# Optimization experiments

Measured on AMD Instinct MI355X. Metric: run time of the kernel, lower is better.

The kernel has to match this reference:

```python
import jax, jax.numpy as jnp
import numpy as np

jax.config.update("jax_enable_x64", True)

N = 100000   # active sparse sites
H = W = 512  # event-camera grid
CIN, CMID, COUT = 64, 384, 64
SHIFT = 16   # shift_n


def setup_inputs() -> dict:
    rng = np.random.default_rng(0)
    # unique active coordinates on the grid (batch index 0)
    flat = rng.permutation(H * W)[:N]
    ys, xs = flat // W, flat % W
    # dense index map with 1-pixel halo; sentinel N = missing neighbor
    idx_map = np.full((H + 2, W + 2), N, dtype=np.int32)
    idx_map[ys + 1, xs + 1] = np.arange(N, dtype=np.int32)
    # 3x3 neighborhood indices per active site, row-major kernel order
    nbr = np.stack([idx_map[ys + 1 + dy, xs + 1 + dx]
                    for dy in (-1, 0, 1) for dx in (-1, 0, 1)], axis=1)

    def ri(lo, hi, shape):
        return jnp.asarray(rng.integers(lo, hi, size=shape), dtype=jnp.float32)

    return {
        "feats": ri(-128, 128, (N, CIN)),      # int8-valued input features
        "w1": ri(-128, 128, (CIN, CMID)),       # 1x1 expand weights
        "b1": ri(-1024, 1024, (CMID,)),
        "s1": ri(1, 16, (CMID,)),
        "w_dw": ri(-128, 128, (9, CMID)),       # 3x3 depthwise weights [k, C]
        "b2": ri(-1024, 1024, (CMID,)),
        "s2": ri(1, 64, (CMID,)),
        "w3": ri(-128, 128, (CMID, COUT)),      # 1x1 project weights
        "b3": ri(-1024, 1024, (COUT,)),
        "s3": ri(1, 16, (COUT,)),
        "neighbor_idx": jnp.asarray(nbr),       # [N, 9] int32, N = sentinel
    }


def _quant(psum, bias, scale, relu):
    # (psum + bias) * scale, add 2^(shift-1), arithmetic >> shift,
    # clamp to int8 range, optional relu. psum values are exact integers.
    t = psum.astype(jnp.int64)
    t = ((t + bias.astype(jnp.int64)) * scale.astype(jnp.int64)
         + (1 << (SHIFT - 1))) >> SHIFT
    y = jnp.clip(t.astype(jnp.float32), -128.0, 127.0)
    return jnp.maximum(y, 0.0) if relu else y


def reference(feats, w1, b1, s1, w_dw, b2, s2, w3, b3, s3, neighbor_idx):
    # 1x1 expand (sparse 1x1 conv == matmul over active sites) + quant + relu
    x1 = _quant(feats @ w1, b1, s1, True)                       # [N, CMID]
    # 3x3 depthwise sparse conv: gather 9 neighbors (zero row for missing)
    pad = jnp.concatenate([x1, jnp.zeros((1, x1.shape[1]), x1.dtype)], axis=0)
    psum2 = jnp.einsum('nkc,kc->nc', pad[neighbor_idx], w_dw)   # [N, CMID]
    x2 = _quant(psum2, b2, s2, True)
    # 1x1 project + quant (linear bottleneck: no relu)
    x3 = _quant(x2 @ w3, b3, s3, False)                          # [N, COUT]
    return x3
```

## Files before the change

### kernel.cpp

```cpp
#include <hip/hip_runtime.h>
#include <stdint.h>

#define N_SITES 100000
#define NPAD    100032
#define CIN 64
#define CMID 384
#define COUT 64
#define SHIFT 16

typedef int  v4i __attribute__((ext_vector_type(4)));
typedef unsigned int v4u __attribute__((ext_vector_type(4)));

__global__ __launch_bounds__(256) void pack_feats(const float* __restrict__ f,
                                                  int8_t* __restrict__ o) {
    int i = blockIdx.x * 256 + threadIdx.x;
    if (i >= N_SITES * CIN / 4) return;
    const float4 v = ((const float4*)f)[i];
    uint32_t w = (uint32_t)(uint8_t)(int8_t)__float2int_rn(v.x)
               | ((uint32_t)(uint8_t)(int8_t)__float2int_rn(v.y) << 8)
               | ((uint32_t)(uint8_t)(int8_t)__float2int_rn(v.z) << 16)
               | ((uint32_t)(uint8_t)(int8_t)__float2int_rn(v.w) << 24);
    ((uint32_t*)o)[i] = w;
}

__global__ __launch_bounds__(256) void pack_weights(
    const float* __restrict__ w1, const float* __restrict__ w3,
    const float* __restrict__ b1, const float* __restrict__ s1,
    const float* __restrict__ b2, const float* __restrict__ s2,
    const float* __restrict__ b3, const float* __restrict__ s3,
    const float* __restrict__ wdw,
    int8_t* __restrict__ w1p, int8_t* __restrict__ w3p,
    int* __restrict__ q1, int* __restrict__ q3,
    int8_t* __restrict__ wdw8, int* __restrict__ bs2,
    int8_t* __restrict__ x1s)
{
    int o = blockIdx.x * 256 + threadIdx.x;
    if (o < 24 * 64 * 16) {
        int t = o >> 10, l = (o >> 4) & 63, b = o & 15;
        int k = ((l >> 4) << 4) + b;
        int col = t * 16 + (l & 15);
        w1p[o] = (int8_t)__float2int_rn(w1[k * CMID + col]);
    }
    int o3 = o - 24 * 64 * 16;
    if (o3 >= 0 && o3 < 6 * 4 * 64 * 16) {
        int ks = o3 >> 12, t = (o3 >> 10) & 3;
        int l = (o3 >> 4) & 63, b = o3 & 15;
        int k = ks * 64 + ((l >> 4) << 4) + b;
        int col = t * 16 + (l & 15);
        w3p[o3] = (int8_t)__float2int_rn(w3[k * COUT + col]);
    }
    if (o < 9 * CMID)
        wdw8[o] = (int8_t)__float2int_rn(wdw[o]);
    if (o < CMID) {
        q1[o] = __float2int_rn(b1[o]);
        q1[CMID + o] = __float2int_rn(s1[o]);
        int bb = __float2int_rn(b2[o]);
        int ss = __float2int_rn(s2[o]);
        bs2[o] = (bb & 0xFFFF) | (ss << 16);
        x1s[(size_t)N_SITES * CMID + o] = 0;
    }
    if (o < COUT) {
        q3[o] = __float2int_rn(b3[o]);
        q3[COUT + o] = __float2int_rn(s3[o]);
    }
}

__global__ __launch_bounds__(256) void k1_mfma(
    const int8_t* __restrict__ feats8, const int8_t* __restrict__ w1p,
    const int* __restrict__ q1, int8_t* __restrict__ x1s)
{
    const int lane = threadIdx.x & 63;
    const int wave = threadIdx.x >> 6;
    const int site0 = blockIdx.x * 64 + wave * 16;
    const int row0 = site0 + ((lane >> 4) << 2);
    const v4i a = *(const v4i*)(feats8 + (size_t)(site0 + (lane & 15)) * CIN
                                + ((lane >> 4) << 4));
    const v4i* bp = (const v4i*)w1p + lane;
#pragma unroll
    for (int t = 0; t < 24; ++t) {
        v4i b = bp[t * 64];
        v4i acc = {0, 0, 0, 0};
        acc = __builtin_amdgcn_mfma_i32_16x16x64_i8(a, b, acc, 0, 0, 0);
        const int col = t * 16 + (lane & 15);
        const int bi = q1[col], si = q1[CMID + col];
#pragma unroll
        for (int r = 0; r < 4; ++r) {
            int site = row0 + r;
            if (site < N_SITES) {
                int v = (acc[r] + bi) * si + (1 << (SHIFT - 1));
                v >>= SHIFT;
                v = max(0, min(127, v));
                x1s[(size_t)site * CMID + col] = (int8_t)v;
            }
        }
    }
}

__global__ __launch_bounds__(256) void k2_dw(
    const int8_t* __restrict__ x1s, const int* __restrict__ nbr,
    const int8_t* __restrict__ wdw8, const int* __restrict__ bs2,
    int8_t* __restrict__ x2s)
{
    const int g = blockIdx.x * 256 + threadIdx.x;
    const int site = g / 24;
    const int c0 = (g - site * 24) << 4;

    const int* nb = &nbr[site * 9];
    int idx[9];
#pragma unroll
    for (int k = 0; k < 9; ++k) idx[k] = nb[k];

    v4u V[9];
#pragma unroll
    for (int k = 0; k < 9; ++k) {
        const int off = (idx[k] << 8) + (idx[k] << 7) + c0;
        V[k] = *(const v4u*)(x1s + off);
    }

    int acc[16];
#pragma unroll
    for (int j = 0; j < 16; ++j) acc[j] = 0;

#pragma unroll
    for (int k = 0; k < 9; ++k) {
        const v4u W = *(const v4u*)(wdw8 + k * CMID + c0);
#pragma unroll
        for (int j = 0; j < 4; ++j) {
#pragma unroll
            for (int b = 0; b < 4; ++b) {
                const int v = (int)(uint8_t)(V[k][j] >> (8 * b));
                const int w = (int)(int8_t)(W[j] >> (8 * b));
                acc[j * 4 + b] += v * w;
            }
        }
    }

    const v4i BS0 = *(const v4i*)(bs2 + c0);
    const v4i BS1 = *(const v4i*)(bs2 + c0 + 4);
    const v4i BS2 = *(const v4i*)(bs2 + c0 + 8);
    const v4i BS3 = *(const v4i*)(bs2 + c0 + 12);
    const v4i BS[4] = {BS0, BS1, BS2, BS3};

    v4u outw;
#pragma unroll
    for (int j = 0; j < 4; ++j) {
        uint32_t wrd = 0;
#pragma unroll
        for (int b = 0; b < 4; ++b) {
            const int bsv = BS[j][b];
            const int bb = (bsv << 16) >> 16;
            const int ss = bsv >> 16;
            int t = ((acc[j * 4 + b] + bb) * ss + (1 << (SHIFT - 1))) >> SHIFT;
            t = max(0, min(127, t));
            wrd |= (uint32_t)t << (8 * b);
        }
        outw[j] = wrd;
    }
    *(v4u*)(x2s + (site << 8) + (site << 7) + c0) = outw;
}

__global__ __launch_bounds__(256) void k3_mfma(
    const int8_t* __restrict__ x2s, const int8_t* __restrict__ w3p,
    const int* __restrict__ q3, float* __restrict__ out)
{
    const int lane = threadIdx.x & 63;
    const int wave = threadIdx.x >> 6;
    const int site0 = blockIdx.x * 64 + wave * 16;
    const int row0 = site0 + ((lane >> 4) << 2);
    const int8_t* xbase = x2s + (size_t)(site0 + (lane & 15)) * CMID
                          + ((lane >> 4) << 4);
    v4i acc[4] = {{0,0,0,0},{0,0,0,0},{0,0,0,0},{0,0,0,0}};
#pragma unroll
    for (int ks = 0; ks < 6; ++ks) {
        v4i a = *(const v4i*)(xbase + ks * 64);
#pragma unroll
        for (int t = 0; t < 4; ++t) {
            v4i b = *((const v4i*)w3p + (ks * 4 + t) * 64 + lane);
            acc[t] = __builtin_amdgcn_mfma_i32_16x16x64_i8(a, b, acc[t], 0, 0, 0);
        }
    }
#pragma unroll
    for (int t = 0; t < 4; ++t) {
        const int col = t * 16 + (lane & 15);
        const int bo = q3[col], so = q3[COUT + col];
#pragma unroll
        for (int r = 0; r < 4; ++r) {
            int site = row0 + r;
            if (site < N_SITES) {
                int v = (acc[t][r] + bo) * so + (1 << (SHIFT - 1));
                v >>= SHIFT;
                v = max(-128, min(127, v));
                out[(size_t)site * COUT + col] = (float)v;
            }
        }
    }
}

extern "C" void kernel_launch(void* const* d_in, const int* in_sizes, int n_in,
                              void* d_out, int out_size, void* d_ws, size_t ws_size,
                              hipStream_t stream) {
    const float* feats = (const float*)d_in[0];
    const float* w1    = (const float*)d_in[1];
    const float* b1    = (const float*)d_in[2];
    const float* s1    = (const float*)d_in[3];
    const float* wdw   = (const float*)d_in[4];
    const float* b2    = (const float*)d_in[5];
    const float* s2    = (const float*)d_in[6];
    const float* w3    = (const float*)d_in[7];
    const float* b3    = (const float*)d_in[8];
    const float* s3    = (const float*)d_in[9];
    const int*   nbr   = (const int*)d_in[10];
    float* out = (float*)d_out;

    int8_t* x1s    = (int8_t*)d_ws;
    int8_t* x2s    = x1s + (size_t)NPAD * CMID;
    int8_t* feats8 = x2s;
    int8_t* w1p    = x2s + (size_t)NPAD * CMID;
    int8_t* w3p    = w1p + 24 * 64 * 16;
    int*    q1     = (int*)(w3p + 6 * 4 * 64 * 16);
    int*    q3     = q1 + 2 * CMID;
    int8_t* wdw8   = (int8_t*)(q3 + 2 * COUT);
    int*    bs2    = (int*)(wdw8 + 9 * CMID);

    pack_feats<<<(N_SITES * CIN / 4 + 255) / 256, 256, 0, stream>>>(feats, feats8);
    pack_weights<<<192, 256, 0, stream>>>(w1, w3, b1, s1, b2, s2, b3, s3, wdw,
                                          w1p, w3p, q1, q3, wdw8, bs2, x1s);
    k1_mfma<<<NPAD / 64, 256, 0, stream>>>(feats8, w1p, q1, x1s);
    k2_dw<<<N_SITES * 24 / 256, 256, 0, stream>>>(x1s, nbr, wdw8, bs2, x2s);
    k3_mfma<<<NPAD / 64, 256, 0, stream>>>(x2s, w3p, q3, out);
}
```

Before: 90.75 us.

## Fuse feature packing into expand GEMM and depthwise into project GEMM via LDS

Removes the separate feature-pack kernel: the expand kernel now reads float features directly, converts them to int8, and swaps the MFMA operand roles so each lane writes packed 4-byte output words instead of single bytes. The depthwise conv and the 1x1 project are fused into one 384-thread kernel. That kernel stages the 64-site x2 tile in shared memory and keeps 4 sites per thread to reuse the depthwise weights, which are now held as int32. This drops the x2 round trip through global memory and one launch, at the cost of higher register pressure and only 4 of 6 waves doing the MFMA phase.

```diff
diff --git a/kernel.cpp b/kernel.cpp
--- a/kernel.cpp
+++ b/kernel.cpp
@@ -8,20 +8,9 @@
 #define COUT 64
 #define SHIFT 16
 
-typedef int  v4i __attribute__((ext_vector_type(4)));
+typedef int   v4i __attribute__((ext_vector_type(4)));
 typedef unsigned int v4u __attribute__((ext_vector_type(4)));
-
-__global__ __launch_bounds__(256) void pack_feats(const float* __restrict__ f,
-                                                  int8_t* __restrict__ o) {
-    int i = blockIdx.x * 256 + threadIdx.x;
-    if (i >= N_SITES * CIN / 4) return;
-    const float4 v = ((const float4*)f)[i];
-    uint32_t w = (uint32_t)(uint8_t)(int8_t)__float2int_rn(v.x)
-               | ((uint32_t)(uint8_t)(int8_t)__float2int_rn(v.y) << 8)
-               | ((uint32_t)(uint8_t)(int8_t)__float2int_rn(v.z) << 16)
-               | ((uint32_t)(uint8_t)(int8_t)__float2int_rn(v.w) << 24);
-    ((uint32_t*)o)[i] = w;
-}
+typedef float v4f __attribute__((ext_vector_type(4)));
 
 __global__ __launch_bounds__(256) void pack_weights(
     const float* __restrict__ w1, const float* __restrict__ w3,
@@ -31,7 +20,7 @@
     const float* __restrict__ wdw,
     int8_t* __restrict__ w1p, int8_t* __restrict__ w3p,
     int* __restrict__ q1, int* __restrict__ q3,
-    int8_t* __restrict__ wdw8, int* __restrict__ bs2,
+    int* __restrict__ wdw32, int* __restrict__ bs2,
     int8_t* __restrict__ x1s)
 {
     int o = blockIdx.x * 256 + threadIdx.x;
@@ -50,7 +39,7 @@
         w3p[o3] = (int8_t)__float2int_rn(w3[k * COUT + col]);
     }
     if (o < 9 * CMID)
-        wdw8[o] = (int8_t)__float2int_rn(wdw[o]);
+        wdw32[o] = __float2int_rn(wdw[o]);
     if (o < CMID) {
         q1[o] = __float2int_rn(b1[o]);
         q1[CMID + o] = __float2int_rn(s1[o]);
@@ -65,132 +54,163 @@
     }
 }
 
-__global__ __launch_bounds__(256) void k1_mfma(
-    const int8_t* __restrict__ feats8, const int8_t* __restrict__ w1p,
+__global__ __launch_bounds__(256) void k1f(
+    const float* __restrict__ feats, const int8_t* __restrict__ w1p,
     const int* __restrict__ q1, int8_t* __restrict__ x1s)
 {
     const int lane = threadIdx.x & 63;
     const int wave = threadIdx.x >> 6;
-    const int site0 = blockIdx.x * 64 + wave * 16;
-    const int row0 = site0 + ((lane >> 4) << 2);
-    const v4i a = *(const v4i*)(feats8 + (size_t)(site0 + (lane & 15)) * CIN
-                                + ((lane >> 4) << 4));
-    const v4i* bp = (const v4i*)w1p + lane;
+    const int site = blockIdx.x * 64 + wave * 16 + (lane & 15);
+    const int rsite = min(site, N_SITES - 1);
+    const bool ok = site < N_SITES;
+    const int kbase = (lane >> 4) << 4;
+    const int cbase = (lane >> 4) << 2;
+
+    v4i b;
+    const float* fp = feats + (size_t)rsite * CIN + kbase;
+#pragma unroll
+    for (int j = 0; j < 4; ++j) {
+        v4f f = *(const v4f*)(fp + 4 * j);
+        uint32_t pk = (uint32_t)(__float2int_rn(f[0]) & 255)
+                    | ((uint32_t)(__float2int_rn(f[1]) & 255) << 8)
+                    | ((uint32_t)(__float2int_rn(f[2]) & 255) << 16)
+                    | ((uint32_t)__float2int_rn(f[3]) << 24);
+        b[j] = (int)pk;
+    }
+
+    const v4i* ap = (const v4i*)w1p + lane;
+    int8_t* orow = x1s + (size_t)site * CMID;
 #pragma unroll
     for (int t = 0; t < 24; ++t) {
-        v4i b = bp[t * 64];
+        v4i a = ap[t * 64];
         v4i acc = {0, 0, 0, 0};
         acc = __builtin_amdgcn_mfma_i32_16x16x64_i8(a, b, acc, 0, 0, 0);
-        const int col = t * 16 + (lane & 15);
-        const int bi = q1[col], si = q1[CMID + col];
+        const int co = t * 16 + cbase;
+        const v4i bi = *(const v4i*)(q1 + co);
+        const v4i si = *(const v4i*)(q1 + CMID + co);
+        uint32_t wrd = 0;
 #pragma unroll
         for (int r = 0; r < 4; ++r) {
-            int site = row0 + r;
-            if (site < N_SITES) {
-                int v = (acc[r] + bi) * si + (1 << (SHIFT - 1));
-                v >>= SHIFT;
-                v = max(0, min(127, v));
-                x1s[(size_t)site * CMID + col] = (int8_t)v;
-            }
-        }
-    }
-}
-
-__global__ __launch_bounds__(256) void k2_dw(
+            int v = (__mul24(acc[r] + bi[r], si[r]) + (1 << (SHIFT - 1))) >> SHIFT;
+            v = max(0, min(127, v));
+            wrd |= (uint32_t)v << (8 * r);
+        }
+        if (ok) *(uint32_t*)(orow + co) = wrd;
+    }
+}
+
+__global__ __launch_bounds__(384) void k23(
     const int8_t* __restrict__ x1s, const int* __restrict__ nbr,
-    const int8_t* __restrict__ wdw8, const int* __restrict__ bs2,
-    int8_t* __restrict__ x2s)
+    const int* __restrict__ wdw32, const int* __restrict__ bs2,
+    const int8_t* __restrict__ w3p, const int* __restrict__ q3,
+    float* __restrict__ out)
 {
-    const int g = blockIdx.x * 256 + threadIdx.x;
-    const int site = g / 24;
-    const int c0 = (g - site * 24) << 4;
-
-    const int* nb = &nbr[site * 9];
-    int idx[9];
-#pragma unroll
-    for (int k = 0; k < 9; ++k) idx[k] = nb[k];
-
-    v4u V[9];
-#pragma unroll
-    for (int k = 0; k < 9; ++k) {
-        const int off = (idx[k] << 8) + (idx[k] << 7) + c0;
-        V[k] = *(const v4u*)(x1s + off);
-    }
-
-    int acc[16];
-#pragma unroll
-    for (int j = 0; j < 16; ++j) acc[j] = 0;
-
-#pragma unroll
-    for (int k = 0; k < 9; ++k) {
-        const v4u W = *(const v4u*)(wdw8 + k * CMID + c0);
-#pragma unroll
-        for (int j = 0; j < 4; ++j) {
-#pragma unroll
-            for (int b = 0; b < 4; ++b) {
-                const int v = (int)(uint8_t)(V[k][j] >> (8 * b));
-                const int w = (int)(int8_t)(W[j] >> (8 * b));
-                acc[j * 4 + b] += v * w;
-            }
-        }
-    }
-
-    const v4i BS0 = *(const v4i*)(bs2 + c0);
-    const v4i BS1 = *(const v4i*)(bs2 + c0 + 4);
-    const v4i BS2 = *(const v4i*)(bs2 + c0 + 8);
-    const v4i BS3 = *(const v4i*)(bs2 + c0 + 12);
-    const v4i BS[4] = {BS0, BS1, BS2, BS3};
-
-    v4u outw;
-#pragma unroll
-    for (int j = 0; j < 4; ++j) {
-        uint32_t wrd = 0;
-#pragma unroll
-        for (int b = 0; b < 4; ++b) {
-            const int bsv = BS[j][b];
-            const int bb = (bsv << 16) >> 16;
-            const int ss = bsv >> 16;
-            int t = ((acc[j * 4 + b] + bb) * ss + (1 << (SHIFT - 1))) >> SHIFT;
-            t = max(0, min(127, t));
-            wrd |= (uint32_t)t << (8 * b);
-        }
-        outw[j] = wrd;
-    }
-    *(v4u*)(x2s + (site << 8) + (site << 7) + c0) = outw;
-}
-
-__global__ __launch_bounds__(256) void k3_mfma(
-    const int8_t* __restrict__ x2s, const int8_t* __restrict__ w3p,
-    const int* __restrict__ q3, float* __restrict__ out)
-{
-    const int lane = threadIdx.x & 63;
-    const int wave = threadIdx.x >> 6;
-    const int site0 = blockIdx.x * 64 + wave * 16;
-    const int row0 = site0 + ((lane >> 4) << 2);
-    const int8_t* xbase = x2s + (size_t)(site0 + (lane & 15)) * CMID
-                          + ((lane >> 4) << 4);
-    v4i acc[4] = {{0,0,0,0},{0,0,0,0},{0,0,0,0},{0,0,0,0}};
-#pragma unroll
-    for (int ks = 0; ks < 6; ++ks) {
-        v4i a = *(const v4i*)(xbase + ks * 64);
-#pragma unroll
-        for (int t = 0; t < 4; ++t) {
-            v4i b = *((const v4i*)w3p + (ks * 4 + t) * 64 + lane);
-            acc[t] = __builtin_amdgcn_mfma_i32_16x16x64_i8(a, b, acc[t], 0, 0, 0);
-        }
-    }
-#pragma unroll
-    for (int t = 0; t < 4; ++t) {
-        const int col = t * 16 + (lane & 15);
-        const int bo = q3[col], so = q3[COUT + col];
-#pragma unroll
-        for (int r = 0; r < 4; ++r) {
-            int site = row0 + r;
-            if (site < N_SITES) {
-                int v = (acc[t][r] + bo) * so + (1 << (SHIFT - 1));
-                v >>= SHIFT;
-                v = max(-128, min(127, v));
-                out[(size_t)site * COUT + col] = (float)v;
+    __shared__ int8_t xt[64][400];
+    const int site0 = blockIdx.x * 64;
+    const int tid = threadIdx.x;
+
+    {
+        const int c0  = (tid % 24) * 16;
+        const int slb = tid / 24;
+
+        int idx[4][9];
+#pragma unroll
+        for (int s = 0; s < 4; ++s) {
+            const int sc = min(site0 + slb + s * 16, N_SITES - 1);
+            const int* nb = nbr + (size_t)sc * 9;
+#pragma unroll
+            for (int k = 0; k < 9; ++k) idx[s][k] = nb[k];
+        }
+
+        int acc[4][16];
+#pragma unroll
+        for (int s = 0; s < 4; ++s)
+#pragma unroll
+            for (int j = 0; j < 16; ++j) acc[s][j] = 0;
+
+#pragma unroll
+        for (int k = 0; k < 9; ++k) {
+            int W[16];
+#pragma unroll
+            for (int j = 0; j < 4; ++j) {
+                v4i w4 = *(const v4i*)(wdw32 + k * CMID + c0 + 4 * j);
+#pragma unroll
+                for (int b = 0; b < 4; ++b) W[j * 4 + b] = w4[b];
+            }
+#pragma unroll
+            for (int s = 0; s < 4; ++s) {
+                const v4u V = *(const v4u*)(x1s + (size_t)idx[s][k] * CMID + c0);
+#pragma unroll
+                for (int j = 0; j < 4; ++j)
+#pragma unroll
+                    for (int b = 0; b < 4; ++b) {
+                        const int v = (int)((V[j] >> (8 * b)) & 0xff);
+                        acc[s][j * 4 + b] += __mul24(v, W[j * 4 + b]);
+                    }
+            }
+        }
+
+        v4i BS[4];
+#pragma unroll
+        for (int j = 0; j < 4; ++j) BS[j] = *(const v4i*)(bs2 + c0 + 4 * j);
+
+#pragma unroll
+        for (int s = 0; s < 4; ++s) {
+            v4u ow;
+#pragma unroll
+            for (int j = 0; j < 4; ++j) {
+                uint32_t wrd = 0;
+#pragma unroll
+                for (int b = 0; b < 4; ++b) {
+                    const int bsv = BS[j][b];
+                    const int bb = (int)(int16_t)(bsv & 0xFFFF);
+                    const int ss = bsv >> 16;
+                    int t = (__mul24(acc[s][j * 4 + b] + bb, ss)
+                             + (1 << (SHIFT - 1))) >> SHIFT;
+                    t = max(0, min(127, t));
+                    wrd |= (uint32_t)t << (8 * b);
+                }
+                ow[j] = wrd;
+            }
+            *(v4u*)(&xt[slb + s * 16][c0]) = ow;
+        }
+    }
+    __syncthreads();
+
+    const int wv = tid >> 6;
+    if (wv < 4) {
+        const int lane = tid & 63;
+        const int sl = wv * 16 + (lane & 15);
+        const int site = site0 + sl;
+        const int kb = (lane >> 4) << 4;
+        const int cb = (lane >> 4) << 2;
+
+        v4i acc3[4] = {{0,0,0,0},{0,0,0,0},{0,0,0,0},{0,0,0,0}};
+#pragma unroll
+        for (int ks = 0; ks < 6; ++ks) {
+            const v4i bfr = *(const v4i*)(&xt[sl][ks * 64 + kb]);
+#pragma unroll
+            for (int t = 0; t < 4; ++t) {
+                const v4i afr = *((const v4i*)w3p + (ks * 4 + t) * 64 + lane);
+                acc3[t] = __builtin_amdgcn_mfma_i32_16x16x64_i8(afr, bfr, acc3[t], 0, 0, 0);
+            }
+        }
+        if (site < N_SITES) {
+            float* orow = out + (size_t)site * COUT;
+#pragma unroll
+            for (int t = 0; t < 4; ++t) {
+                const int co = t * 16 + cb;
+                const v4i bo = *(const v4i*)(q3 + co);
+                const v4i so = *(const v4i*)(q3 + COUT + co);
+                v4f o;
+#pragma unroll
+                for (int r = 0; r < 4; ++r) {
+                    int v = (__mul24(acc3[t][r] + bo[r], so[r])
+                             + (1 << (SHIFT - 1))) >> SHIFT;
+                    v = max(-128, min(127, v));
+                    o[r] = (float)v;
+                }
+                *(v4f*)(orow + co) = o;
             }
         }
     }
@@ -212,20 +232,16 @@
     const int*   nbr   = (const int*)d_in[10];
     float* out = (float*)d_out;
 
-    int8_t* x1s    = (int8_t*)d_ws;
-    int8_t* x2s    = x1s + (size_t)NPAD * CMID;
-    int8_t* feats8 = x2s;
-    int8_t* w1p    = x2s + (size_t)NPAD * CMID;
-    int8_t* w3p    = w1p + 24 * 64 * 16;
-    int*    q1     = (int*)(w3p + 6 * 4 * 64 * 16);
-    int*    q3     = q1 + 2 * CMID;
-    int8_t* wdw8   = (int8_t*)(q3 + 2 * COUT);
-    int*    bs2    = (int*)(wdw8 + 9 * CMID);
-
-    pack_feats<<<(N_SITES * CIN / 4 + 255) / 256, 256, 0, stream>>>(feats, feats8);
+    int8_t* x1s   = (int8_t*)d_ws;
+    int8_t* w1p   = x1s + (size_t)(NPAD + 64) * CMID;
+    int8_t* w3p   = w1p + 24 * 64 * 16;
+    int*    q1    = (int*)(w3p + 6 * 4 * 64 * 16);
+    int*    q3    = q1 + 2 * CMID;
+    int*    wdw32 = q3 + 2 * COUT;
+    int*    bs2   = wdw32 + 9 * CMID;
+
     pack_weights<<<192, 256, 0, stream>>>(w1, w3, b1, s1, b2, s2, b3, s3, wdw,
-                                          w1p, w3p, q1, q3, wdw8, bs2, x1s);
-    k1_mfma<<<NPAD / 64, 256, 0, stream>>>(feats8, w1p, q1, x1s);
-    k2_dw<<<N_SITES * 24 / 256, 256, 0, stream>>>(x1s, nbr, wdw8, bs2, x2s);
-    k3_mfma<<<NPAD / 64, 256, 0, stream>>>(x2s, w3p, q3, out);
-}
+                                          w1p, w3p, q1, q3, wdw32, bs2, x1s);
+    k1f<<<NPAD / 64, 256, 0, stream>>>(feats, w1p, q1, x1s);
+    k23<<<NPAD / 64, 384, 0, stream>>>(x1s, nbr, wdw32, bs2, w3p, q3, out);
+}
```

Result: slower. 122.8 us (+35.3%).

## Merge pack kernels and use packed sdot4 in depthwise kernel

Applied to the files above, without the earlier changes.

Folds the feature-packing and weight-packing kernels into a single launch, removing one kernel launch and its gap. The depthwise kernel now keeps its weights pre-packed four taps per word. It uses byte permutes plus sdot4 to do four neighbor multiply-adds per instruction instead of scalar byte-extract multiplies. Bias and scale are stored unpacked, and __mul24 is used for the requantize step. This adds dependence on sdot4 builtin availability, with a scalar fallback, and relies on x1 values being non-negative int8 for signed dot correctness.

```diff
diff --git a/kernel.cpp b/kernel.cpp
--- a/kernel.cpp
+++ b/kernel.cpp
@@ -8,33 +8,43 @@
 #define COUT 64
 #define SHIFT 16
 
-typedef int  v4i __attribute__((ext_vector_type(4)));
+#define FEAT_BLOCKS 6250
+
+typedef int   v4i __attribute__((ext_vector_type(4)));
 typedef unsigned int v4u __attribute__((ext_vector_type(4)));
 
-__global__ __launch_bounds__(256) void pack_feats(const float* __restrict__ f,
-                                                  int8_t* __restrict__ o) {
-    int i = blockIdx.x * 256 + threadIdx.x;
-    if (i >= N_SITES * CIN / 4) return;
-    const float4 v = ((const float4*)f)[i];
-    uint32_t w = (uint32_t)(uint8_t)(int8_t)__float2int_rn(v.x)
-               | ((uint32_t)(uint8_t)(int8_t)__float2int_rn(v.y) << 8)
-               | ((uint32_t)(uint8_t)(int8_t)__float2int_rn(v.z) << 16)
-               | ((uint32_t)(uint8_t)(int8_t)__float2int_rn(v.w) << 24);
-    ((uint32_t*)o)[i] = w;
-}
-
-__global__ __launch_bounds__(256) void pack_weights(
+#if __has_builtin(__builtin_amdgcn_sdot4)
+#define HAS_SDOT4 1
+#else
+#define HAS_SDOT4 0
+#endif
+
+__global__ __launch_bounds__(256) void pack_all(
+    const float* __restrict__ feats,
     const float* __restrict__ w1, const float* __restrict__ w3,
     const float* __restrict__ b1, const float* __restrict__ s1,
     const float* __restrict__ b2, const float* __restrict__ s2,
     const float* __restrict__ b3, const float* __restrict__ s3,
     const float* __restrict__ wdw,
+    int8_t* __restrict__ feats8,
     int8_t* __restrict__ w1p, int8_t* __restrict__ w3p,
     int* __restrict__ q1, int* __restrict__ q3,
-    int8_t* __restrict__ wdw8, int* __restrict__ bs2,
+    int* __restrict__ wp03, int* __restrict__ wp47, int* __restrict__ w8,
+    int* __restrict__ q2b, int* __restrict__ q2s,
     int8_t* __restrict__ x1s)
 {
-    int o = blockIdx.x * 256 + threadIdx.x;
+    if (blockIdx.x < FEAT_BLOCKS) {
+        int i = blockIdx.x * 256 + threadIdx.x;
+        if (i >= N_SITES * CIN / 4) return;
+        const float4 v = ((const float4*)feats)[i];
+        uint32_t w = (uint32_t)(uint8_t)(int8_t)__float2int_rn(v.x)
+                   | ((uint32_t)(uint8_t)(int8_t)__float2int_rn(v.y) << 8)
+                   | ((uint32_t)(uint8_t)(int8_t)__float2int_rn(v.z) << 16)
+                   | ((uint32_t)(uint8_t)(int8_t)__float2int_rn(v.w) << 24);
+        ((uint32_t*)feats8)[i] = w;
+        return;
+    }
+    int o = (blockIdx.x - FEAT_BLOCKS) * 256 + threadIdx.x;
     if (o < 24 * 64 * 16) {
         int t = o >> 10, l = (o >> 4) & 63, b = o & 15;
         int k = ((l >> 4) << 4) + b;
@@ -49,14 +59,21 @@
         int col = t * 16 + (l & 15);
         w3p[o3] = (int8_t)__float2int_rn(w3[k * COUT + col]);
     }
-    if (o < 9 * CMID)
-        wdw8[o] = (int8_t)__float2int_rn(wdw[o]);
     if (o < CMID) {
+        uint32_t p03 = 0, p47 = 0;
+#pragma unroll
+        for (int k = 0; k < 4; ++k)
+            p03 |= (uint32_t)(uint8_t)(int8_t)__float2int_rn(wdw[k * CMID + o]) << (8 * k);
+#pragma unroll
+        for (int k = 0; k < 4; ++k)
+            p47 |= (uint32_t)(uint8_t)(int8_t)__float2int_rn(wdw[(k + 4) * CMID + o]) << (8 * k);
+        wp03[o] = (int)p03;
+        wp47[o] = (int)p47;
+        w8[o]   = __float2int_rn(wdw[8 * CMID + o]);
+        q2b[o]  = __float2int_rn(b2[o]);
+        q2s[o]  = __float2int_rn(s2[o]);
         q1[o] = __float2int_rn(b1[o]);
         q1[CMID + o] = __float2int_rn(s1[o]);
-        int bb = __float2int_rn(b2[o]);
-        int ss = __float2int_rn(s2[o]);
-        bs2[o] = (bb & 0xFFFF) | (ss << 16);
         x1s[(size_t)N_SITES * CMID + o] = 0;
     }
     if (o < COUT) {
@@ -98,65 +115,69 @@
 
 __global__ __launch_bounds__(256) void k2_dw(
     const int8_t* __restrict__ x1s, const int* __restrict__ nbr,
-    const int8_t* __restrict__ wdw8, const int* __restrict__ bs2,
-    int8_t* __restrict__ x2s)
+    const int* __restrict__ wp03, const int* __restrict__ wp47,
+    const int* __restrict__ w8, const int* __restrict__ q2b,
+    const int* __restrict__ q2s, int8_t* __restrict__ x2s)
 {
     const int g = blockIdx.x * 256 + threadIdx.x;
     const int site = g / 24;
     const int c0 = (g - site * 24) << 4;
 
-    const int* nb = &nbr[site * 9];
+    const int* nb = nbr + (size_t)site * 9;
     int idx[9];
 #pragma unroll
     for (int k = 0; k < 9; ++k) idx[k] = nb[k];
 
     v4u V[9];
 #pragma unroll
-    for (int k = 0; k < 9; ++k) {
-        const int off = (idx[k] << 8) + (idx[k] << 7) + c0;
-        V[k] = *(const v4u*)(x1s + off);
-    }
-
-    int acc[16];
-#pragma unroll
-    for (int j = 0; j < 16; ++j) acc[j] = 0;
-
-#pragma unroll
-    for (int k = 0; k < 9; ++k) {
-        const v4u W = *(const v4u*)(wdw8 + k * CMID + c0);
-#pragma unroll
-        for (int j = 0; j < 4; ++j) {
-#pragma unroll
-            for (int b = 0; b < 4; ++b) {
-                const int v = (int)(uint8_t)(V[k][j] >> (8 * b));
-                const int w = (int)(int8_t)(W[j] >> (8 * b));
-                acc[j * 4 + b] += v * w;
-            }
-        }
-    }
-
-    const v4i BS0 = *(const v4i*)(bs2 + c0);
-    const v4i BS1 = *(const v4i*)(bs2 + c0 + 4);
-    const v4i BS2 = *(const v4i*)(bs2 + c0 + 8);
-    const v4i BS3 = *(const v4i*)(bs2 + c0 + 12);
-    const v4i BS[4] = {BS0, BS1, BS2, BS3};
+    for (int k = 0; k < 9; ++k)
+        V[k] = *(const v4u*)(x1s + (size_t)idx[k] * CMID + c0);
 
     v4u outw;
 #pragma unroll
     for (int j = 0; j < 4; ++j) {
+        const v4i wa  = *(const v4i*)(wp03 + c0 + 4 * j);
+        const v4i wb  = *(const v4i*)(wp47 + c0 + 4 * j);
+        const v4i w8v = *(const v4i*)(w8   + c0 + 4 * j);
+        const v4i bb  = *(const v4i*)(q2b  + c0 + 4 * j);
+        const v4i ss  = *(const v4i*)(q2s  + c0 + 4 * j);
         uint32_t wrd = 0;
 #pragma unroll
         for (int b = 0; b < 4; ++b) {
-            const int bsv = BS[j][b];
-            const int bb = (bsv << 16) >> 16;
-            const int ss = bsv >> 16;
-            int t = ((acc[j * 4 + b] + bb) * ss + (1 << (SHIFT - 1))) >> SHIFT;
+            const int v8 = (int)((V[8][j] >> (8 * b)) & 0xff);
+            int acc = v8 * w8v[b];
+#if HAS_SDOT4
+            const unsigned selA = (unsigned)b | ((unsigned)(4 + b) << 4);
+            const unsigned selB = ((unsigned)b << 8) | ((unsigned)(4 + b) << 12);
+            unsigned t01 = __byte_perm(V[0][j], V[1][j], selA);
+            unsigned t23 = __byte_perm(V[2][j], V[3][j], selB);
+            unsigned a03 = __byte_perm(t01, t23, 0x7610);
+            unsigned u01 = __byte_perm(V[4][j], V[5][j], selA);
+            unsigned u23 = __byte_perm(V[6][j], V[7][j], selB);
+            unsigned a47 = __byte_perm(u01, u23, 0x7610);
+            acc = __builtin_amdgcn_sdot4((int)a03, wa[b], acc, false);
+            acc = __builtin_amdgcn_sdot4((int)a47, wb[b], acc, false);
+#else
+#pragma unroll
+            for (int k = 0; k < 4; ++k) {
+                const int v = (int)((V[k][j] >> (8 * b)) & 0xff);
+                const int w = ((int)wa[b] << (24 - 8 * k)) >> 24;
+                acc += v * w;
+            }
+#pragma unroll
+            for (int k = 0; k < 4; ++k) {
+                const int v = (int)((V[k + 4][j] >> (8 * b)) & 0xff);
+                const int w = ((int)wb[b] << (24 - 8 * k)) >> 24;
+                acc += v * w;
+            }
+#endif
+            int t = (__mul24(acc + bb[b], ss[b]) + (1 << (SHIFT - 1))) >> SHIFT;
             t = max(0, min(127, t));
             wrd |= (uint32_t)t << (8 * b);
         }
         outw[j] = wrd;
     }
-    *(v4u*)(x2s + (site << 8) + (site << 7) + c0) = outw;
+    *(v4u*)(x2s + (size_t)site * CMID + c0) = outw;
 }
 
 __global__ __launch_bounds__(256) void k3_mfma(
@@ -219,13 +240,17 @@
     int8_t* w3p    = w1p + 24 * 64 * 16;
     int*    q1     = (int*)(w3p + 6 * 4 * 64 * 16);
     int*    q3     = q1 + 2 * CMID;
-    int8_t* wdw8   = (int8_t*)(q3 + 2 * COUT);
-    int*    bs2    = (int*)(wdw8 + 9 * CMID);
-
-    pack_feats<<<(N_SITES * CIN / 4 + 255) / 256, 256, 0, stream>>>(feats, feats8);
-    pack_weights<<<192, 256, 0, stream>>>(w1, w3, b1, s1, b2, s2, b3, s3, wdw,
-                                          w1p, w3p, q1, q3, wdw8, bs2, x1s);
+    int*    wp03   = q3 + 2 * COUT;
+    int*    wp47   = wp03 + CMID;
+    int*    w8     = wp47 + CMID;
+    int*    q2b    = w8 + CMID;
+    int*    q2s    = q2b + CMID;
+
+    pack_all<<<FEAT_BLOCKS + 192, 256, 0, stream>>>(
+        feats, w1, w3, b1, s1, b2, s2, b3, s3, wdw,
+        feats8, w1p, w3p, q1, q3, wp03, wp47, w8, q2b, q2s, x1s);
     k1_mfma<<<NPAD / 64, 256, 0, stream>>>(feats8, w1p, q1, x1s);
-    k2_dw<<<N_SITES * 24 / 256, 256, 0, stream>>>(x1s, nbr, wdw8, bs2, x2s);
+    k2_dw<<<N_SITES * 24 / 256, 256, 0, stream>>>(x1s, nbr, wp03, wp47, w8,
+                                                  q2b, q2s, x2s);
     k3_mfma<<<NPAD / 64, 256, 0, stream>>>(x2s, w3p, q3, out);
 }
```

Result: slower. 110.2 us (+21.4%).

## Transpose MFMA operands for packed row stores and merge pack kernels

Applied to the files above, without the earlier changes.

Swaps the A and B operands of the int8 MFMA in the expand and project kernels, so each lane holds four consecutive output channels of one site. This lets x1 be written as packed 32-bit words and the output as float4 vectors instead of scattered single-byte and single-float stores, with bias and scale loaded as vectors. It also merges the feature-pack and weight-pack kernels into one launch to save a kernel launch. The operand swap relies on the existing weight packing layout staying valid when used as the A fragment.

```diff
diff --git a/kernel.cpp b/kernel.cpp
--- a/kernel.cpp
+++ b/kernel.cpp
@@ -8,33 +8,37 @@
 #define COUT 64
 #define SHIFT 16
 
-typedef int  v4i __attribute__((ext_vector_type(4)));
+#define FEAT_BLOCKS 6250
+
+typedef int   v4i __attribute__((ext_vector_type(4)));
 typedef unsigned int v4u __attribute__((ext_vector_type(4)));
-
-__global__ __launch_bounds__(256) void pack_feats(const float* __restrict__ f,
-                                                  int8_t* __restrict__ o) {
-    int i = blockIdx.x * 256 + threadIdx.x;
-    if (i >= N_SITES * CIN / 4) return;
-    const float4 v = ((const float4*)f)[i];
-    uint32_t w = (uint32_t)(uint8_t)(int8_t)__float2int_rn(v.x)
-               | ((uint32_t)(uint8_t)(int8_t)__float2int_rn(v.y) << 8)
-               | ((uint32_t)(uint8_t)(int8_t)__float2int_rn(v.z) << 16)
-               | ((uint32_t)(uint8_t)(int8_t)__float2int_rn(v.w) << 24);
-    ((uint32_t*)o)[i] = w;
-}
-
-__global__ __launch_bounds__(256) void pack_weights(
+typedef float v4f __attribute__((ext_vector_type(4)));
+
+__global__ __launch_bounds__(256) void pack_all(
+    const float* __restrict__ feats,
     const float* __restrict__ w1, const float* __restrict__ w3,
     const float* __restrict__ b1, const float* __restrict__ s1,
     const float* __restrict__ b2, const float* __restrict__ s2,
     const float* __restrict__ b3, const float* __restrict__ s3,
     const float* __restrict__ wdw,
+    int8_t* __restrict__ feats8,
     int8_t* __restrict__ w1p, int8_t* __restrict__ w3p,
     int* __restrict__ q1, int* __restrict__ q3,
     int8_t* __restrict__ wdw8, int* __restrict__ bs2,
     int8_t* __restrict__ x1s)
 {
-    int o = blockIdx.x * 256 + threadIdx.x;
+    if (blockIdx.x < FEAT_BLOCKS) {
+        int i = blockIdx.x * 256 + threadIdx.x;
+        if (i >= N_SITES * CIN / 4) return;
+        const float4 v = ((const float4*)feats)[i];
+        uint32_t w = (uint32_t)(uint8_t)(int8_t)__float2int_rn(v.x)
+                   | ((uint32_t)(uint8_t)(int8_t)__float2int_rn(v.y) << 8)
+                   | ((uint32_t)(uint8_t)(int8_t)__float2int_rn(v.z) << 16)
+                   | ((uint32_t)(uint8_t)(int8_t)__float2int_rn(v.w) << 24);
+        ((uint32_t*)feats8)[i] = w;
+        return;
+    }
+    int o = (blockIdx.x - FEAT_BLOCKS) * 256 + threadIdx.x;
     if (o < 24 * 64 * 16) {
         int t = o >> 10, l = (o >> 4) & 63, b = o & 15;
         int k = ((l >> 4) << 4) + b;
@@ -71,28 +75,29 @@
 {
     const int lane = threadIdx.x & 63;
     const int wave = threadIdx.x >> 6;
-    const int site0 = blockIdx.x * 64 + wave * 16;
-    const int row0 = site0 + ((lane >> 4) << 2);
-    const v4i a = *(const v4i*)(feats8 + (size_t)(site0 + (lane & 15)) * CIN
-                                + ((lane >> 4) << 4));
-    const v4i* bp = (const v4i*)w1p + lane;
+    const int site = blockIdx.x * 64 + wave * 16 + (lane & 15);
+    const bool ok = site < N_SITES;
+    const int cb = (lane >> 4) << 2;
+
+    const v4i b = *(const v4i*)(feats8 + (size_t)site * CIN + ((lane >> 4) << 4));
+    const v4i* ap = (const v4i*)w1p + lane;
+    int8_t* orow = x1s + (size_t)site * CMID;
 #pragma unroll
     for (int t = 0; t < 24; ++t) {
-        v4i b = bp[t * 64];
+        v4i a = ap[t * 64];
         v4i acc = {0, 0, 0, 0};
         acc = __builtin_amdgcn_mfma_i32_16x16x64_i8(a, b, acc, 0, 0, 0);
-        const int col = t * 16 + (lane & 15);
-        const int bi = q1[col], si = q1[CMID + col];
+        const int co = t * 16 + cb;
+        const v4i bi = *(const v4i*)(q1 + co);
+        const v4i si = *(const v4i*)(q1 + CMID + co);
+        uint32_t wrd = 0;
 #pragma unroll
         for (int r = 0; r < 4; ++r) {
-            int site = row0 + r;
-            if (site < N_SITES) {
-                int v = (acc[r] + bi) * si + (1 << (SHIFT - 1));
-                v >>= SHIFT;
-                v = max(0, min(127, v));
-                x1s[(size_t)site * CMID + col] = (int8_t)v;
-            }
-        }
+            int v = ((acc[r] + bi[r]) * si[r] + (1 << (SHIFT - 1))) >> SHIFT;
+            v = max(0, min(127, v));
+            wrd |= (uint32_t)v << (8 * r);
+        }
+        if (ok) *(uint32_t*)(orow + co) = wrd;
     }
 }
 
@@ -165,33 +170,35 @@
 {
     const int lane = threadIdx.x & 63;
     const int wave = threadIdx.x >> 6;
-    const int site0 = blockIdx.x * 64 + wave * 16;
-    const int row0 = site0 + ((lane >> 4) << 2);
-    const int8_t* xbase = x2s + (size_t)(site0 + (lane & 15)) * CMID
-                          + ((lane >> 4) << 4);
+    const int site = blockIdx.x * 64 + wave * 16 + (lane & 15);
+    const int cb = (lane >> 4) << 2;
+    const int8_t* xrow = x2s + (size_t)site * CMID + ((lane >> 4) << 4);
+
     v4i acc[4] = {{0,0,0,0},{0,0,0,0},{0,0,0,0},{0,0,0,0}};
 #pragma unroll
     for (int ks = 0; ks < 6; ++ks) {
-        v4i a = *(const v4i*)(xbase + ks * 64);
+        const v4i bfr = *(const v4i*)(xrow + ks * 64);
 #pragma unroll
         for (int t = 0; t < 4; ++t) {
-            v4i b = *((const v4i*)w3p + (ks * 4 + t) * 64 + lane);
-            acc[t] = __builtin_amdgcn_mfma_i32_16x16x64_i8(a, b, acc[t], 0, 0, 0);
-        }
-    }
-#pragma unroll
-    for (int t = 0; t < 4; ++t) {
-        const int col = t * 16 + (lane & 15);
-        const int bo = q3[col], so = q3[COUT + col];
-#pragma unroll
-        for (int r = 0; r < 4; ++r) {
-            int site = row0 + r;
-            if (site < N_SITES) {
-                int v = (acc[t][r] + bo) * so + (1 << (SHIFT - 1));
-                v >>= SHIFT;
+            const v4i afr = *((const v4i*)w3p + (ks * 4 + t) * 64 + lane);
+            acc[t] = __builtin_amdgcn_mfma_i32_16x16x64_i8(afr, bfr, acc[t], 0, 0, 0);
+        }
+    }
+    if (site < N_SITES) {
+        float* orow = out + (size_t)site * COUT;
+#pragma unroll
+        for (int t = 0; t < 4; ++t) {
+            const int co = t * 16 + cb;
+            const v4i bo = *(const v4i*)(q3 + co);
+            const v4i so = *(const v4i*)(q3 + COUT + co);
+            v4f o;
+#pragma unroll
+            for (int r = 0; r < 4; ++r) {
+                int v = ((acc[t][r] + bo[r]) * so[r] + (1 << (SHIFT - 1))) >> SHIFT;
                 v = max(-128, min(127, v));
-                out[(size_t)site * COUT + col] = (float)v;
+                o[r] = (float)v;
             }
+            *(v4f*)(orow + co) = o;
         }
     }
 }
@@ -222,9 +229,9 @@
     int8_t* wdw8   = (int8_t*)(q3 + 2 * COUT);
     int*    bs2    = (int*)(wdw8 + 9 * CMID);
 
-    pack_feats<<<(N_SITES * CIN / 4 + 255) / 256, 256, 0, stream>>>(feats, feats8);
-    pack_weights<<<192, 256, 0, stream>>>(w1, w3, b1, s1, b2, s2, b3, s3, wdw,
-                                          w1p, w3p, q1, q3, wdw8, bs2, x1s);
+    pack_all<<<FEAT_BLOCKS + 192, 256, 0, stream>>>(
+        feats, w1, w3, b1, s1, b2, s2, b3, s3, wdw,
+        feats8, w1p, w3p, q1, q3, wdw8, bs2, x1s);
     k1_mfma<<<NPAD / 64, 256, 0, stream>>>(feats8, w1p, q1, x1s);
     k2_dw<<<N_SITES * 24 / 256, 256, 0, stream>>>(x1s, nbr, wdw8, bs2, x2s);
     k3_mfma<<<NPAD / 64, 256, 0, stream>>>(x2s, w3p, q3, out);
```

After: 100.2 us. 1.1x slower.
